# Kernel optimization log

Hardware: AMD Instinct MI355X
Metric: run time of the kernel (lower is better)

Reference implementation:

```python
import jax, jax.numpy as jnp
import numpy as np

N_NODES = 50000

def _gat_conv(x, src, dst, W, a_src, a_dst, bias, num_nodes, concat, neg_slope=0.2):
    # x: [N, Fin]; W: [Fin, H*C]; a_src/a_dst: [H, C]; src/dst: [E]
    H, C = a_src.shape
    h = (x @ W).reshape(-1, H, C)                      # [N, H, C]
    alpha_s = jnp.einsum('nhc,hc->nh', h, a_src)        # [N, H]
    alpha_d = jnp.einsum('nhc,hc->nh', h, a_dst)        # [N, H]
    e = alpha_s[src] + alpha_d[dst]                     # [E, H]
    e = jax.nn.leaky_relu(e, neg_slope)
    # segment softmax over destination nodes
    m = jax.ops.segment_max(e, dst, num_segments=num_nodes)   # [N, H]
    ex = jnp.exp(e - m[dst])                                   # [E, H]
    denom = jax.ops.segment_sum(ex, dst, num_segments=num_nodes)  # [N, H]
    alpha = ex / denom[dst]                                    # [E, H]
    msg = h[src] * alpha[:, :, None]                            # [E, H, C]
    out = jax.ops.segment_sum(msg, dst, num_segments=num_nodes)  # [N, H, C]
    if concat:
        out = out.reshape(-1, H * C)
    else:
        out = out.mean(axis=1)
    return out + bias

def _add_self_loops(edge_index, num_nodes):
    loop = jnp.arange(num_nodes, dtype=edge_index.dtype)
    src = jnp.concatenate([edge_index[0], loop])
    dst = jnp.concatenate([edge_index[1], loop])
    return src, dst

def setup_inputs() -> dict:
    key = jax.random.key(0)
    ks = jax.random.split(key, 12)
    N, E = N_NODES, 800000
    in_c, hid, out_c, H = 128, 32, 64, 4
    x = jax.random.normal(ks[0], (N, in_c), dtype=jnp.float32)
    edge_index = jax.random.randint(ks[1], (2, E), 0, N, dtype=jnp.int64)
    edge_weight = jax.random.uniform(ks[2], (E,), dtype=jnp.float32)
    s1 = 1.0 / np.sqrt(in_c)
    s2 = 1.0 / np.sqrt(hid * H)
    W1 = jax.random.normal(ks[3], (in_c, H * hid), dtype=jnp.float32) * s1
    a_src1 = jax.random.normal(ks[4], (H, hid), dtype=jnp.float32) * s1
    a_dst1 = jax.random.normal(ks[5], (H, hid), dtype=jnp.float32) * s1
    b1 = jnp.zeros((H * hid,), dtype=jnp.float32)
    W2 = jax.random.normal(ks[6], (H * hid, out_c), dtype=jnp.float32) * s2
    a_src2 = jax.random.normal(ks[7], (1, out_c), dtype=jnp.float32) * s2
    a_dst2 = jax.random.normal(ks[8], (1, out_c), dtype=jnp.float32) * s2
    b2 = jnp.zeros((out_c,), dtype=jnp.float32)
    return {"x": x, "edge_index": edge_index, "edge_weight": edge_weight,
            "W1": W1, "a_src1": a_src1, "a_dst1": a_dst1, "b1": b1,
            "W2": W2, "a_src2": a_src2, "a_dst2": a_dst2, "b2": b2}

def reference(x, edge_index, edge_weight, W1, a_src1, a_dst1, b1, W2, a_src2, a_dst2, b2):
    # PyG GATConv with edge_dim unset ignores edge_weight; self-loops added by default
    N = x.shape[0]
    src, dst = _add_self_loops(edge_index, N)
    h = _gat_conv(x, src, dst, W1, a_src1, a_dst1, b1, N, concat=True)
    h = jax.nn.relu(h)
    out = _gat_conv(h, src, dst, W2, a_src2, a_dst2, b2, N, concat=False)
    return out
```

## Files before the change

kernel.cpp:

```cpp
#include <hip/hip_runtime.h>
#include <hip/hip_fp16.h>
#include <math.h>


#define NEG_SLOPE 0.2f
#define NBLKA 256
#define MAXNB 512

__device__ __forceinline__ float leaky(float v) { return v > 0.f ? v : NEG_SLOPE * v; }

__global__ __launch_bounds__(256) void histc_k(const int* __restrict__ ei, int E, int ET,
                                               int* __restrict__ blkpref, int NB) {
  __shared__ int lhist[MAXNB];
  int chunk = (ET + NBLKA - 1) / NBLKA;
  int e0 = blockIdx.x * chunk, e1 = min(ET, e0 + chunk);
  for (int b = threadIdx.x; b < NB; b += 256) lhist[b] = 0;
  __syncthreads();
  for (int e = e0 + threadIdx.x; e < e1; e += 256) {
    int d = (e < E) ? ei[E + e] : (e - E);
    atomicAdd(&lhist[d >> 7], 1);
  }
  __syncthreads();
  for (int b = threadIdx.x; b < NB; b += 256)
    blkpref[b * NBLKA + blockIdx.x] = lhist[b];
}

__global__ __launch_bounds__(256) void scan_blk_k(int* __restrict__ blkpref,
                                                  int* __restrict__ bbase) {
  __shared__ int sm[NBLKA];
  int b = blockIdx.x, t = threadIdx.x;
  int v = blkpref[b * NBLKA + t];
  sm[t] = v;
  __syncthreads();
  #pragma unroll
  for (int off = 1; off < NBLKA; off <<= 1) {
    int x = (t >= off) ? sm[t - off] : 0;
    __syncthreads();
    sm[t] += x;
    __syncthreads();
  }
  blkpref[b * NBLKA + t] = sm[t] - v;
  if (t == NBLKA - 1) bbase[b] = sm[t];
}

__global__ __launch_bounds__(512) void scan_bkt_k(int* __restrict__ bbase,
                                                  int* __restrict__ lcnt,
                                                  int* __restrict__ rowptr,
                                                  int NB, int N, int ET) {
  __shared__ int sm[512];
  int t = threadIdx.x;
  int v = (t < NB) ? bbase[t] : 0;
  sm[t] = v;
  __syncthreads();
  #pragma unroll
  for (int off = 1; off < 512; off <<= 1) {
    int x = (t >= off) ? sm[t - off] : 0;
    __syncthreads();
    sm[t] += x;
    __syncthreads();
  }
  int excl = sm[t] - v;
  if (t <= NB) bbase[t] = excl;
  if (t == 0) { lcnt[0] = 0; lcnt[16] = 0; rowptr[N] = ET; }
}

__global__ __launch_bounds__(256) void passA_k(const int* __restrict__ ei, int E, int ET,
                                               const int* __restrict__ bbase,
                                               const int* __restrict__ blkpref,
                                               int* __restrict__ pairs, int NB) {
  __shared__ int lcur[MAXNB];
  int chunk = (ET + NBLKA - 1) / NBLKA;
  int e0 = blockIdx.x * chunk, e1 = min(ET, e0 + chunk);
  for (int b = threadIdx.x; b < NB; b += 256)
    lcur[b] = bbase[b] + blkpref[b * NBLKA + blockIdx.x];
  __syncthreads();
  for (int e = e0 + threadIdx.x; e < e1; e += 256) {
    int s, d;
    if (e < E) { s = ei[e]; d = ei[E + e]; } else { s = d = e - E; }
    int b = d >> 7;
    int pos = atomicAdd(&lcur[b], 1);
    pairs[pos] = ((d & 127) << 17) | s;
  }
}

__global__ __launch_bounds__(256) void passB_k(const int* __restrict__ pairs,
                                               const int* __restrict__ bbase,
                                               int* __restrict__ rowptr,
                                               int* __restrict__ srcs,
                                               int* __restrict__ small_list,
                                               int* __restrict__ big_list,
                                               int* __restrict__ lcnt, int N) {
  __shared__ int ncnt[128], spre[128], lcur[128];
  __shared__ int wcS[2], wcB[2], bS, bB;
  int b = blockIdx.x, t = threadIdx.x;
  int nb0 = b << 7;
  int nn = min(128, N - nb0);
  int e0 = bbase[b], e1 = bbase[b + 1];
  if (t < 128) ncnt[t] = 0;
  __syncthreads();
  for (int r = e0 + t; r < e1; r += 256)
    atomicAdd(&ncnt[pairs[r] >> 17], 1);
  __syncthreads();
  if (t < 128) spre[t] = ncnt[t];
  __syncthreads();
  #pragma unroll
  for (int off = 1; off < 128; off <<= 1) {
    int x = (t < 128 && t >= off) ? spre[t - off] : 0;
    __syncthreads();
    if (t < 128) spre[t] += x;
    __syncthreads();
  }
  if (t < nn) {
    int base = e0 + spre[t] - ncnt[t];
    rowptr[nb0 + t] = base;
    lcur[t] = base;
  }
  __syncthreads();
  for (int r = e0 + t; r < e1; r += 256) {
    int p = pairs[r];
    int pos = atomicAdd(&lcur[p >> 17], 1);
    srcs[pos] = p & 0x1FFFF;
  }
  int lane = t & 63, wv = t >> 6;
  bool valid = (t < nn);
  int deg = valid ? ncnt[t] : 0;
  bool isS = valid && (deg <= 16);
  bool isB = valid && (deg > 16);
  unsigned long long ms = __ballot(isS);
  unsigned long long mb = __ballot(isB);
  if (lane == 0 && wv < 2) { wcS[wv] = __popcll(ms); wcB[wv] = __popcll(mb); }
  __syncthreads();
  if (t == 0) {
    bS = atomicAdd(&lcnt[0],  wcS[0] + wcS[1]);
    bB = atomicAdd(&lcnt[16], wcB[0] + wcB[1]);
  }
  __syncthreads();
  unsigned long long below = (lane == 0) ? 0ull : (~0ull >> (64 - lane));
  int offS = bS + ((wv == 1) ? wcS[0] : 0);
  int offB = bB + ((wv == 1) ? wcB[0] : 0);
  if (isS) small_list[offS + __popcll(ms & below)] = nb0 + t;
  if (isB) big_list[offB + __popcll(mb & below)]   = nb0 + t;
}

__global__ __launch_bounds__(256) void gemm1_k(const float* __restrict__ X,
                                               const float* __restrict__ W,
                                               const float* __restrict__ aw_s,
                                               const float* __restrict__ aw_d,
                                               __half* __restrict__ Hh,
                                               float* __restrict__ as,
                                               float* __restrict__ ad, int N) {
  __shared__ float wl[32 * 128];
  __shared__ float xt[32][72];
  int cl = threadIdx.x & 31, rg = threadIdx.x >> 5;
  int c4 = cl * 4;
  int n0 = blockIdx.x * 64;
  float acc[8][4] = {};
  const float4* X4 = (const float4*)X;
  const float4* W4 = (const float4*)W;
  for (int k0 = 0; k0 < 128; k0 += 32) {
    __syncthreads();
    for (int i = threadIdx.x; i < 1024; i += 256)
      ((float4*)wl)[i] = W4[k0 * 32 + i];
    for (int i = threadIdx.x; i < 512; i += 256) {
      int r = i >> 3, kk4 = (i & 7) * 4;
      int n = n0 + r;
      float4 xv = (n < N) ? X4[(size_t)n * 32 + (k0 >> 2) + (i & 7)]
                          : make_float4(0.f, 0.f, 0.f, 0.f);
      xt[kk4 + 0][r] = xv.x; xt[kk4 + 1][r] = xv.y;
      xt[kk4 + 2][r] = xv.z; xt[kk4 + 3][r] = xv.w;
    }
    __syncthreads();
    #pragma unroll 8
    for (int kk = 0; kk < 32; ++kk) {
      float4 w4 = *(const float4*)&wl[kk * 128 + c4];
      float4 xa = *(const float4*)&xt[kk][rg * 8];
      float4 xb = *(const float4*)&xt[kk][rg * 8 + 4];
      float xr[8] = {xa.x, xa.y, xa.z, xa.w, xb.x, xb.y, xb.z, xb.w};
      #pragma unroll
      for (int j = 0; j < 8; ++j) {
        acc[j][0] += xr[j] * w4.x; acc[j][1] += xr[j] * w4.y;
        acc[j][2] += xr[j] * w4.z; acc[j][3] += xr[j] * w4.w;
      }
    }
  }
  float4 aws = *(const float4*)&aw_s[c4];
  float4 awd = *(const float4*)&aw_d[c4];
  #pragma unroll
  for (int j = 0; j < 8; ++j) {
    int n = n0 + rg * 8 + j;
    float ps = acc[j][0] * aws.x + acc[j][1] * aws.y + acc[j][2] * aws.z + acc[j][3] * aws.w;
    float pd = acc[j][0] * awd.x + acc[j][1] * awd.y + acc[j][2] * awd.z + acc[j][3] * awd.w;
    ps += __shfl_xor(ps, 1); ps += __shfl_xor(ps, 2); ps += __shfl_xor(ps, 4);
    pd += __shfl_xor(pd, 1); pd += __shfl_xor(pd, 2); pd += __shfl_xor(pd, 4);
    if (n < N) {
      __half2 p0 = __floats2half2_rn(acc[j][0], acc[j][1]);
      __half2 p1 = __floats2half2_rn(acc[j][2], acc[j][3]);
      __half2* dst = (__half2*)&Hh[(size_t)n * 128 + c4];
      dst[0] = p0; dst[1] = p1;
      if ((cl & 7) == 0) {
        as[n * 4 + (cl >> 3)] = ps;
        ad[n * 4 + (cl >> 3)] = pd;
      }
    }
  }
}

__global__ __launch_bounds__(256) void gemm2_k(const float* __restrict__ X,
                                               const float* __restrict__ W,
                                               const float* __restrict__ aw_s,
                                               const float* __restrict__ aw_d,
                                               __half* __restrict__ Hh,
                                               float* __restrict__ as,
                                               float* __restrict__ ad, int N) {
  __shared__ float wl[32 * 64];
  __shared__ float xt[32][72];
  int cl = threadIdx.x & 15, rg = threadIdx.x >> 4;
  int c4 = cl * 4;
  int n0 = blockIdx.x * 64;
  float acc[4][4] = {};
  const float4* X4 = (const float4*)X;
  const float4* W4 = (const float4*)W;
  for (int k0 = 0; k0 < 128; k0 += 32) {
    __syncthreads();
    for (int i = threadIdx.x; i < 512; i += 256)
      ((float4*)wl)[i] = W4[k0 * 16 + i];
    for (int i = threadIdx.x; i < 512; i += 256) {
      int r = i >> 3, kk4 = (i & 7) * 4;
      int n = n0 + r;
      float4 xv = (n < N) ? X4[(size_t)n * 32 + (k0 >> 2) + (i & 7)]
                          : make_float4(0.f, 0.f, 0.f, 0.f);
      xt[kk4 + 0][r] = xv.x; xt[kk4 + 1][r] = xv.y;
      xt[kk4 + 2][r] = xv.z; xt[kk4 + 3][r] = xv.w;
    }
    __syncthreads();
    #pragma unroll 8
    for (int kk = 0; kk < 32; ++kk) {
      float4 w4 = *(const float4*)&wl[kk * 64 + c4];
      float4 xa = *(const float4*)&xt[kk][rg * 4];
      float xr[4] = {xa.x, xa.y, xa.z, xa.w};
      #pragma unroll
      for (int j = 0; j < 4; ++j) {
        acc[j][0] += xr[j] * w4.x; acc[j][1] += xr[j] * w4.y;
        acc[j][2] += xr[j] * w4.z; acc[j][3] += xr[j] * w4.w;
      }
    }
  }
  float4 aws = *(const float4*)&aw_s[c4];
  float4 awd = *(const float4*)&aw_d[c4];
  #pragma unroll
  for (int j = 0; j < 4; ++j) {
    int n = n0 + rg * 4 + j;
    float ps = acc[j][0] * aws.x + acc[j][1] * aws.y + acc[j][2] * aws.z + acc[j][3] * aws.w;
    float pd = acc[j][0] * awd.x + acc[j][1] * awd.y + acc[j][2] * awd.z + acc[j][3] * awd.w;
    ps += __shfl_xor(ps, 1); ps += __shfl_xor(ps, 2);
    ps += __shfl_xor(ps, 4); ps += __shfl_xor(ps, 8);
    pd += __shfl_xor(pd, 1); pd += __shfl_xor(pd, 2);
    pd += __shfl_xor(pd, 4); pd += __shfl_xor(pd, 8);
    if (n < N) {
      __half2 p0 = __floats2half2_rn(acc[j][0], acc[j][1]);
      __half2 p1 = __floats2half2_rn(acc[j][2], acc[j][3]);
      __half2* dst = (__half2*)&Hh[(size_t)n * 64 + c4];
      dst[0] = p0; dst[1] = p1;
      if (cl == 0) { as[n] = ps; ad[n] = pd; }
    }
  }
}

__device__ __forceinline__ void load8h(const __half* p, float* f) {
  uint4 hv = *(const uint4*)p;
  float2 f0 = __half22float2(*(const __half2*)&hv.x);
  float2 f1 = __half22float2(*(const __half2*)&hv.y);
  float2 f2 = __half22float2(*(const __half2*)&hv.z);
  float2 f3 = __half22float2(*(const __half2*)&hv.w);
  f[0] = f0.x; f[1] = f0.y; f[2] = f1.x; f[3] = f1.y;
  f[4] = f2.x; f[5] = f2.y; f[6] = f3.x; f[7] = f3.y;
}

__global__ __launch_bounds__(256) void agg1_small_k(const int* __restrict__ rowptr,
                                                    const int* __restrict__ srcs,
                                                    const float* __restrict__ as,
                                                    const float* __restrict__ ad,
                                                    const __half* __restrict__ Hm,
                                                    const float* __restrict__ bias,
                                                    float* __restrict__ out,
                                                    const int* __restrict__ small_list,
                                                    const int* __restrict__ lcnt) {
  __shared__ float al_sm[16][17][4];
  __shared__ int   sr_sm[16][16];
  int g  = threadIdx.x >> 4;
  int gl = threadIdx.x & 15;
  int gidx = blockIdx.x * 16 + g;
  if (gidx >= lcnt[0]) return;
  int n = small_list[gidx];
  int r0 = rowptr[n];
  int deg = rowptr[n + 1] - r0;
  float4 adn = *(const float4*)&ad[n * 4];

  float e0 = -INFINITY, e1 = -INFINITY, e2 = -INFINITY, e3 = -INFINITY;
  int s = 0;
  if (gl < deg) {
    s = srcs[r0 + gl];
    float4 av = *(const float4*)&as[s * 4];
    e0 = leaky(av.x + adn.x); e1 = leaky(av.y + adn.y);
    e2 = leaky(av.z + adn.z); e3 = leaky(av.w + adn.w);
  }
  sr_sm[g][gl] = s;
  float m0 = e0, m1 = e1, m2 = e2, m3 = e3;
  #pragma unroll
  for (int off = 8; off > 0; off >>= 1) {
    m0 = fmaxf(m0, __shfl_xor(m0, off, 16)); m1 = fmaxf(m1, __shfl_xor(m1, off, 16));
    m2 = fmaxf(m2, __shfl_xor(m2, off, 16)); m3 = fmaxf(m3, __shfl_xor(m3, off, 16));
  }
  float sc0 = (gl < deg) ? __expf(e0 - m0) : 0.f;
  float sc1 = (gl < deg) ? __expf(e1 - m1) : 0.f;
  float sc2 = (gl < deg) ? __expf(e2 - m2) : 0.f;
  float sc3 = (gl < deg) ? __expf(e3 - m3) : 0.f;
  float s0 = sc0, s1 = sc1, s2 = sc2, s3 = sc3;
  #pragma unroll
  for (int off = 8; off > 0; off >>= 1) {
    s0 += __shfl_xor(s0, off, 16); s1 += __shfl_xor(s1, off, 16);
    s2 += __shfl_xor(s2, off, 16); s3 += __shfl_xor(s3, off, 16);
  }
  *(float4*)&al_sm[g][gl][0] =
      make_float4(sc0 / s0, sc1 / s1, sc2 / s2, sc3 / s3);

  int h = gl >> 2;
  int cbase = gl * 8;
  float a0 = 0.f, a1 = 0.f, a2 = 0.f, a3 = 0.f,
        a4 = 0.f, a5 = 0.f, a6 = 0.f, a7 = 0.f;
  for (int j = 0; j < deg; j += 4) {
    #pragma unroll
    for (int u = 0; u < 4; ++u) {
      int idx = j + u;
      bool vU = idx < deg;
      int jj = vU ? idx : 0;
      int   sU  = sr_sm[g][jj];
      float alU = vU ? al_sm[g][jj][h] : 0.f;
      float f[8];
      load8h(&Hm[(size_t)sU * 128 + cbase], f);
      a0 += f[0] * alU; a1 += f[1] * alU; a2 += f[2] * alU; a3 += f[3] * alU;
      a4 += f[4] * alU; a5 += f[5] * alU; a6 += f[6] * alU; a7 += f[7] * alU;
    }
  }
  float4 b0 = *(const float4*)&bias[cbase];
  float4 b1 = *(const float4*)&bias[cbase + 4];
  float4 o0, o1;
  o0.x = fmaxf(a0 + b0.x, 0.f); o0.y = fmaxf(a1 + b0.y, 0.f);
  o0.z = fmaxf(a2 + b0.z, 0.f); o0.w = fmaxf(a3 + b0.w, 0.f);
  o1.x = fmaxf(a4 + b1.x, 0.f); o1.y = fmaxf(a5 + b1.y, 0.f);
  o1.z = fmaxf(a6 + b1.z, 0.f); o1.w = fmaxf(a7 + b1.w, 0.f);
  *(float4*)&out[(size_t)n * 128 + cbase] = o0;
  *(float4*)&out[(size_t)n * 128 + cbase + 4] = o1;
}

__global__ __launch_bounds__(256) void agg1_big_k(const int* __restrict__ rowptr,
                                                  const int* __restrict__ srcs,
                                                  const float* __restrict__ as,
                                                  const float* __restrict__ ad,
                                                  const __half* __restrict__ Hm,
                                                  const float* __restrict__ bias,
                                                  float* __restrict__ out,
                                                  const int* __restrict__ big_list,
                                                  const int* __restrict__ lcnt) {
  __shared__ float al_sm[4][64][4];
  __shared__ int   sr_sm[4][64];
  int wv = threadIdx.x >> 6, lane = threadIdx.x & 63;
  int widx = blockIdx.x * 4 + wv;
  if (widx >= lcnt[16]) return;
  int n = big_list[widx];
  int r0 = rowptr[n], r1 = rowptr[n + 1];
  int deg = r1 - r0;
  int grp = lane >> 4, gl = lane & 15, h = gl >> 2;
  int cbase = gl * 8;
  float4 adn = *(const float4*)&ad[n * 4];

  float a0 = 0.f, a1 = 0.f, a2 = 0.f, a3 = 0.f,
        a4 = 0.f, a5 = 0.f, a6 = 0.f, a7 = 0.f;

  if (deg <= 64) {
    float e0 = -INFINITY, e1 = -INFINITY, e2 = -INFINITY, e3 = -INFINITY;
    int s = 0;
    if (lane < deg) {
      s = srcs[r0 + lane];
      float4 av = *(const float4*)&as[s * 4];
      e0 = leaky(av.x + adn.x); e1 = leaky(av.y + adn.y);
      e2 = leaky(av.z + adn.z); e3 = leaky(av.w + adn.w);
    }
    sr_sm[wv][lane] = s;
    float m0 = e0, m1 = e1, m2 = e2, m3 = e3;
    #pragma unroll
    for (int off = 32; off > 0; off >>= 1) {
      m0 = fmaxf(m0, __shfl_xor(m0, off)); m1 = fmaxf(m1, __shfl_xor(m1, off));
      m2 = fmaxf(m2, __shfl_xor(m2, off)); m3 = fmaxf(m3, __shfl_xor(m3, off));
    }
    float sc0 = (lane < deg) ? __expf(e0 - m0) : 0.f;
    float sc1 = (lane < deg) ? __expf(e1 - m1) : 0.f;
    float sc2 = (lane < deg) ? __expf(e2 - m2) : 0.f;
    float sc3 = (lane < deg) ? __expf(e3 - m3) : 0.f;
    float s0 = sc0, s1 = sc1, s2 = sc2, s3 = sc3;
    #pragma unroll
    for (int off = 32; off > 0; off >>= 1) {
      s0 += __shfl_xor(s0, off); s1 += __shfl_xor(s1, off);
      s2 += __shfl_xor(s2, off); s3 += __shfl_xor(s3, off);
    }
    *(float4*)&al_sm[wv][lane][0] =
        make_float4(sc0 / s0, sc1 / s1, sc2 / s2, sc3 / s3);

    for (int base = 0; base < deg; base += 16) {
      #pragma unroll
      for (int u = 0; u < 4; ++u) {
        int idx = base + grp * 4 + u;
        bool vU = idx < deg;
        int jj = vU ? idx : 0;
        int   sU  = sr_sm[wv][jj];
        float alU = vU ? al_sm[wv][jj][h] : 0.f;
        float f[8];
        load8h(&Hm[(size_t)sU * 128 + cbase], f);
        a0 += f[0] * alU; a1 += f[1] * alU; a2 += f[2] * alU; a3 += f[3] * alU;
        a4 += f[4] * alU; a5 += f[5] * alU; a6 += f[6] * alU; a7 += f[7] * alU;
      }
    }
  } else {
    float m0 = -INFINITY, m1 = -INFINITY, m2 = -INFINITY, m3 = -INFINITY;
    for (int r = r0 + lane; r < r1; r += 64) {
      int s = srcs[r];
      float4 av = *(const float4*)&as[s * 4];
      m0 = fmaxf(m0, leaky(av.x + adn.x)); m1 = fmaxf(m1, leaky(av.y + adn.y));
      m2 = fmaxf(m2, leaky(av.z + adn.z)); m3 = fmaxf(m3, leaky(av.w + adn.w));
    }
    #pragma unroll
    for (int off = 32; off > 0; off >>= 1) {
      m0 = fmaxf(m0, __shfl_xor(m0, off)); m1 = fmaxf(m1, __shfl_xor(m1, off));
      m2 = fmaxf(m2, __shfl_xor(m2, off)); m3 = fmaxf(m3, __shfl_xor(m3, off));
    }
    float s0 = 0.f, s1 = 0.f, s2 = 0.f, s3 = 0.f;
    for (int r = r0 + lane; r < r1; r += 64) {
      int s = srcs[r];
      float4 av = *(const float4*)&as[s * 4];
      s0 += __expf(leaky(av.x + adn.x) - m0); s1 += __expf(leaky(av.y + adn.y) - m1);
      s2 += __expf(leaky(av.z + adn.z) - m2); s3 += __expf(leaky(av.w + adn.w) - m3);
    }
    #pragma unroll
    for (int off = 32; off > 0; off >>= 1) {
      s0 += __shfl_xor(s0, off); s1 += __shfl_xor(s1, off);
      s2 += __shfl_xor(s2, off); s3 += __shfl_xor(s3, off);
    }
    float mhh = (h == 0) ? m0 : (h == 1) ? m1 : (h == 2) ? m2 : m3;
    float inv = 1.f / ((h == 0) ? s0 : (h == 1) ? s1 : (h == 2) ? s2 : s3);
    float adh = (h == 0) ? adn.x : (h == 1) ? adn.y : (h == 2) ? adn.z : adn.w;
    for (int r = r0; r < r1; r += 8) {
      int rA = r + grp, rB = rA + 4;
      bool vA = rA < r1, vB = rB < r1;
      int sA = srcs[vA ? rA : r0];
      int sB = srcs[vB ? rB : r0];
      float avA = as[sA * 4 + h], avB = as[sB * 4 + h];
      float alA = vA ? (__expf(leaky(avA + adh) - mhh) * inv) : 0.f;
      float alB = vB ? (__expf(leaky(avB + adh) - mhh) * inv) : 0.f;
      float fA[8], fB[8];
      load8h(&Hm[(size_t)sA * 128 + cbase], fA);
      load8h(&Hm[(size_t)sB * 128 + cbase], fB);
      a0 += fA[0] * alA + fB[0] * alB; a1 += fA[1] * alA + fB[1] * alB;
      a2 += fA[2] * alA + fB[2] * alB; a3 += fA[3] * alA + fB[3] * alB;
      a4 += fA[4] * alA + fB[4] * alB; a5 += fA[5] * alA + fB[5] * alB;
      a6 += fA[6] * alA + fB[6] * alB; a7 += fA[7] * alA + fB[7] * alB;
    }
  }
  a0 += __shfl_xor(a0, 16); a0 += __shfl_xor(a0, 32);
  a1 += __shfl_xor(a1, 16); a1 += __shfl_xor(a1, 32);
  a2 += __shfl_xor(a2, 16); a2 += __shfl_xor(a2, 32);
  a3 += __shfl_xor(a3, 16); a3 += __shfl_xor(a3, 32);
  a4 += __shfl_xor(a4, 16); a4 += __shfl_xor(a4, 32);
  a5 += __shfl_xor(a5, 16); a5 += __shfl_xor(a5, 32);
  a6 += __shfl_xor(a6, 16); a6 += __shfl_xor(a6, 32);
  a7 += __shfl_xor(a7, 16); a7 += __shfl_xor(a7, 32);
  if (grp == 0) {
    float4 b0 = *(const float4*)&bias[cbase];
    float4 b1 = *(const float4*)&bias[cbase + 4];
    float4 o0, o1;
    o0.x = fmaxf(a0 + b0.x, 0.f); o0.y = fmaxf(a1 + b0.y, 0.f);
    o0.z = fmaxf(a2 + b0.z, 0.f); o0.w = fmaxf(a3 + b0.w, 0.f);
    o1.x = fmaxf(a4 + b1.x, 0.f); o1.y = fmaxf(a5 + b1.y, 0.f);
    o1.z = fmaxf(a6 + b1.z, 0.f); o1.w = fmaxf(a7 + b1.w, 0.f);
    *(float4*)&out[(size_t)n * 128 + cbase] = o0;
    *(float4*)&out[(size_t)n * 128 + cbase + 4] = o1;
  }
}

__global__ __launch_bounds__(256) void agg2_small_k(const int* __restrict__ rowptr,
                                                    const int* __restrict__ srcs,
                                                    const float* __restrict__ as,
                                                    const float* __restrict__ ad,
                                                    const __half* __restrict__ Hm,
                                                    const float* __restrict__ bias,
                                                    float* __restrict__ out,
                                                    const int* __restrict__ small_list,
                                                    const int* __restrict__ lcnt) {
  __shared__ float al_sm[16][17];
  __shared__ int   sr_sm[16][16];
  int g  = threadIdx.x >> 4;
  int gl = threadIdx.x & 15;
  int gidx = blockIdx.x * 16 + g;
  if (gidx >= lcnt[0]) return;
  int n = small_list[gidx];
  int r0 = rowptr[n];
  int deg = rowptr[n + 1] - r0;
  float adn = ad[n];

  float e = -INFINITY;
  int s = 0;
  if (gl < deg) { s = srcs[r0 + gl]; e = leaky(as[s] + adn); }
  sr_sm[g][gl] = s;
  float m = e;
  #pragma unroll
  for (int off = 8; off > 0; off >>= 1) m = fmaxf(m, __shfl_xor(m, off, 16));
  float sc = (gl < deg) ? __expf(e - m) : 0.f;
  float ssum = sc;
  #pragma unroll
  for (int off = 8; off > 0; off >>= 1) ssum += __shfl_xor(ssum, off, 16);
  al_sm[g][gl] = sc / ssum;

  int cbase = gl * 4;
  float a0 = 0.f, a1 = 0.f, a2 = 0.f, a3 = 0.f;
  for (int j = 0; j < deg; j += 4) {
    #pragma unroll
    for (int u = 0; u < 4; ++u) {
      int idx = j + u;
      bool vU = idx < deg;
      int jj = vU ? idx : 0;
      int   sU  = sr_sm[g][jj];
      float alU = vU ? al_sm[g][jj] : 0.f;
      uint2 hv = *(const uint2*)&Hm[(size_t)sU * 64 + cbase];
      float2 f0 = __half22float2(*(const __half2*)&hv.x);
      float2 f1 = __half22float2(*(const __half2*)&hv.y);
      a0 += f0.x * alU; a1 += f0.y * alU; a2 += f1.x * alU; a3 += f1.y * alU;
    }
  }
  float4 bv = *(const float4*)&bias[cbase];
  float4 o;
  o.x = a0 + bv.x; o.y = a1 + bv.y; o.z = a2 + bv.z; o.w = a3 + bv.w;
  *(float4*)&out[(size_t)n * 64 + cbase] = o;
}

__global__ __launch_bounds__(256) void agg2_big_k(const int* __restrict__ rowptr,
                                                  const int* __restrict__ srcs,
                                                  const float* __restrict__ as,
                                                  const float* __restrict__ ad,
                                                  const __half* __restrict__ Hm,
                                                  const float* __restrict__ bias,
                                                  float* __restrict__ out,
                                                  const int* __restrict__ big_list,
                                                  const int* __restrict__ lcnt) {
  __shared__ float al_sm[4][64];
  __shared__ int   sr_sm[4][64];
  int wv = threadIdx.x >> 6, lane = threadIdx.x & 63;
  int widx = blockIdx.x * 4 + wv;
  if (widx >= lcnt[16]) return;
  int n = big_list[widx];
  int r0 = rowptr[n], r1 = rowptr[n + 1];
  int deg = r1 - r0;
  int grp = lane >> 4, gl = lane & 15;
  int cbase = gl * 4;
  float adn = ad[n];

  float a0 = 0.f, a1 = 0.f, a2 = 0.f, a3 = 0.f;

  if (deg <= 64) {
    float e = -INFINITY;
    int s = 0;
    if (lane < deg) { s = srcs[r0 + lane]; e = leaky(as[s] + adn); }
    sr_sm[wv][lane] = s;
    float m = e;
    #pragma unroll
    for (int off = 32; off > 0; off >>= 1) m = fmaxf(m, __shfl_xor(m, off));
    float sc = (lane < deg) ? __expf(e - m) : 0.f;
    float ssum = sc;
    #pragma unroll
    for (int off = 32; off > 0; off >>= 1) ssum += __shfl_xor(ssum, off);
    al_sm[wv][lane] = sc / ssum;

    for (int base = 0; base < deg; base += 16) {
      #pragma unroll
      for (int u = 0; u < 4; ++u) {
        int idx = base + grp * 4 + u;
        bool vU = idx < deg;
        int jj = vU ? idx : 0;
        int   sU  = sr_sm[wv][jj];
        float alU = vU ? al_sm[wv][jj] : 0.f;
        uint2 hv = *(const uint2*)&Hm[(size_t)sU * 64 + cbase];
        float2 f0 = __half22float2(*(const __half2*)&hv.x);
        float2 f1 = __half22float2(*(const __half2*)&hv.y);
        a0 += f0.x * alU; a1 += f0.y * alU; a2 += f1.x * alU; a3 += f1.y * alU;
      }
    }
  } else {
    float mh = -INFINITY;
    for (int r = r0 + lane; r < r1; r += 64)
      mh = fmaxf(mh, leaky(as[srcs[r]] + adn));
    #pragma unroll
    for (int off = 32; off > 0; off >>= 1) mh = fmaxf(mh, __shfl_xor(mh, off));
    float ssum = 0.f;
    for (int r = r0 + lane; r < r1; r += 64)
      ssum += __expf(leaky(as[srcs[r]] + adn) - mh);
    #pragma unroll
    for (int off = 32; off > 0; off >>= 1) ssum += __shfl_xor(ssum, off);
    float inv = 1.f / ssum;
    for (int r = r0; r < r1; r += 8) {
      int rA = r + grp, rB = rA + 4;
      bool vA = rA < r1, vB = rB < r1;
      int sA = srcs[vA ? rA : r0];
      int sB = srcs[vB ? rB : r0];
      float alA = vA ? (__expf(leaky(as[sA] + adn) - mh) * inv) : 0.f;
      float alB = vB ? (__expf(leaky(as[sB] + adn) - mh) * inv) : 0.f;
      uint2 hvA = *(const uint2*)&Hm[(size_t)sA * 64 + cbase];
      uint2 hvB = *(const uint2*)&Hm[(size_t)sB * 64 + cbase];
      float2 fA0 = __half22float2(*(const __half2*)&hvA.x);
      float2 fA1 = __half22float2(*(const __half2*)&hvA.y);
      float2 fB0 = __half22float2(*(const __half2*)&hvB.x);
      float2 fB1 = __half22float2(*(const __half2*)&hvB.y);
      a0 += fA0.x * alA + fB0.x * alB; a1 += fA0.y * alA + fB0.y * alB;
      a2 += fA1.x * alA + fB1.x * alB; a3 += fA1.y * alA + fB1.y * alB;
    }
  }
  a0 += __shfl_xor(a0, 16); a0 += __shfl_xor(a0, 32);
  a1 += __shfl_xor(a1, 16); a1 += __shfl_xor(a1, 32);
  a2 += __shfl_xor(a2, 16); a2 += __shfl_xor(a2, 32);
  a3 += __shfl_xor(a3, 16); a3 += __shfl_xor(a3, 32);
  if (grp == 0) {
    float4 bv = *(const float4*)&bias[cbase];
    float4 o;
    o.x = a0 + bv.x; o.y = a1 + bv.y; o.z = a2 + bv.z; o.w = a3 + bv.w;
    *(float4*)&out[(size_t)n * 64 + cbase] = o;
  }
}

extern "C" void kernel_launch(void* const* d_in, const int* in_sizes, int n_in,
                              void* d_out, int out_size, void* d_ws, size_t ws_size,
                              hipStream_t stream) {
  const float* x   = (const float*)d_in[0];
  const int*   ei  = (const int*)d_in[1];
  const float* W1  = (const float*)d_in[3];
  const float* aS1 = (const float*)d_in[4];
  const float* aD1 = (const float*)d_in[5];
  const float* b1  = (const float*)d_in[6];
  const float* W2  = (const float*)d_in[7];
  const float* aS2 = (const float*)d_in[8];
  const float* aD2 = (const float*)d_in[9];
  const float* b2  = (const float*)d_in[10];

  const int N  = in_sizes[0] / 128;
  const int E  = in_sizes[2];
  const int ET = E + N;
  const int NB = (N + 127) >> 7;

  float* ws   = (float*)d_ws;
  __half* h1h = (__half*)ws;
  float* out1 = ws + (size_t)N * 64;
  float* as1  = out1 + (size_t)N * 128;
  float* ad1  = as1  + (size_t)4 * N;
  float* as2  = ad1  + (size_t)4 * N;
  float* ad2  = as2  + (size_t)N;
  int*   lcnt    = (int*)(ad2 + (size_t)N);
  int*   rowptr  = lcnt + 32;
  int*   bbase   = rowptr + N + 1;
  int*   blkpref = bbase + NB + 1;
  int*   small_list = blkpref + NB * NBLKA;
  int*   big_list   = small_list + N;
  int*   srcs   = big_list + N;
  int*   pairs  = (int*)ws;
  __half* h2h  = h1h;
  float* out  = (float*)d_out;

  const int gb  = (N + 63) / 64;
  const int sb  = (N + 15) / 16;
  const int bb  = (N + 3) / 4;

  histc_k<<<NBLKA, 256, 0, stream>>>(ei, E, ET, blkpref, NB);
  scan_blk_k<<<NB, 256, 0, stream>>>(blkpref, bbase);
  scan_bkt_k<<<1, 512, 0, stream>>>(bbase, lcnt, rowptr, NB, N, ET);
  passA_k<<<NBLKA, 256, 0, stream>>>(ei, E, ET, bbase, blkpref, pairs, NB);
  passB_k<<<NB, 256, 0, stream>>>(pairs, bbase, rowptr, srcs,
                                  small_list, big_list, lcnt, N);

  gemm1_k<<<gb, 256, 0, stream>>>(x, W1, aS1, aD1, h1h, as1, ad1, N);
  agg1_small_k<<<sb, 256, 0, stream>>>(rowptr, srcs, as1, ad1, h1h, b1, out1,
                                       small_list, lcnt);
  agg1_big_k<<<bb, 256, 0, stream>>>(rowptr, srcs, as1, ad1, h1h, b1, out1,
                                     big_list, lcnt);

  gemm2_k<<<gb, 256, 0, stream>>>(out1, W2, aS2, aD2, h2h, as2, ad2, N);
  agg2_small_k<<<sb, 256, 0, stream>>>(rowptr, srcs, as2, ad2, h2h, b2, out,
                                       small_list, lcnt);
  agg2_big_k<<<bb, 256, 0, stream>>>(rowptr, srcs, as2, ad2, h2h, b2, out,
                                     big_list, lcnt);
}
```

Baseline: 243.9 us.

## Merge small/big aggregation kernels and store layer-1 output in fp16

The separate small-degree and big-degree aggregation kernels for each layer are merged into one launch, with blocks below SB taking the small path and the rest the big path. This removes two kernel launches and lets both node classes run at the same time. The layer-1 activation is now written as fp16 and read back by gemm2 as fp16, which halves that intermediate's write and read traffic at some cost in precision.

```diff
diff --git a/kernel.cpp b/kernel.cpp
--- a/kernel.cpp
+++ b/kernel.cpp
@@ -193,10 +193,9 @@
     ps += __shfl_xor(ps, 1); ps += __shfl_xor(ps, 2); ps += __shfl_xor(ps, 4);
     pd += __shfl_xor(pd, 1); pd += __shfl_xor(pd, 2); pd += __shfl_xor(pd, 4);
     if (n < N) {
-      __half2 p0 = __floats2half2_rn(acc[j][0], acc[j][1]);
-      __half2 p1 = __floats2half2_rn(acc[j][2], acc[j][3]);
       __half2* dst = (__half2*)&Hh[(size_t)n * 128 + c4];
-      dst[0] = p0; dst[1] = p1;
+      dst[0] = __floats2half2_rn(acc[j][0], acc[j][1]);
+      dst[1] = __floats2half2_rn(acc[j][2], acc[j][3]);
       if ((cl & 7) == 0) {
         as[n * 4 + (cl >> 3)] = ps;
         ad[n * 4 + (cl >> 3)] = pd;
@@ -205,7 +204,7 @@
   }
 }
 
-__global__ __launch_bounds__(256) void gemm2_k(const float* __restrict__ X,
+__global__ __launch_bounds__(256) void gemm2_k(const __half* __restrict__ X,
                                                const float* __restrict__ W,
                                                const float* __restrict__ aw_s,
                                                const float* __restrict__ aw_d,
@@ -218,19 +217,25 @@
   int c4 = cl * 4;
   int n0 = blockIdx.x * 64;
   float acc[4][4] = {};
-  const float4* X4 = (const float4*)X;
+  const uint4* X8 = (const uint4*)X;
   const float4* W4 = (const float4*)W;
   for (int k0 = 0; k0 < 128; k0 += 32) {
     __syncthreads();
     for (int i = threadIdx.x; i < 512; i += 256)
       ((float4*)wl)[i] = W4[k0 * 16 + i];
-    for (int i = threadIdx.x; i < 512; i += 256) {
-      int r = i >> 3, kk4 = (i & 7) * 4;
+    for (int i = threadIdx.x; i < 256; i += 256) {
+      int r = i >> 2, kk8 = (i & 3) * 8;
       int n = n0 + r;
-      float4 xv = (n < N) ? X4[(size_t)n * 32 + (k0 >> 2) + (i & 7)]
-                          : make_float4(0.f, 0.f, 0.f, 0.f);
-      xt[kk4 + 0][r] = xv.x; xt[kk4 + 1][r] = xv.y;
-      xt[kk4 + 2][r] = xv.z; xt[kk4 + 3][r] = xv.w;
+      uint4 hv = (n < N) ? X8[(size_t)n * 16 + (k0 >> 3) + (i & 3)]
+                         : make_uint4(0, 0, 0, 0);
+      float2 f0 = __half22float2(*(const __half2*)&hv.x);
+      float2 f1 = __half22float2(*(const __half2*)&hv.y);
+      float2 f2 = __half22float2(*(const __half2*)&hv.z);
+      float2 f3 = __half22float2(*(const __half2*)&hv.w);
+      xt[kk8 + 0][r] = f0.x; xt[kk8 + 1][r] = f0.y;
+      xt[kk8 + 2][r] = f1.x; xt[kk8 + 3][r] = f1.y;
+      xt[kk8 + 4][r] = f2.x; xt[kk8 + 5][r] = f2.y;
+      xt[kk8 + 6][r] = f3.x; xt[kk8 + 7][r] = f3.y;
     }
     __syncthreads();
     #pragma unroll 8
@@ -257,10 +262,9 @@
     pd += __shfl_xor(pd, 1); pd += __shfl_xor(pd, 2);
     pd += __shfl_xor(pd, 4); pd += __shfl_xor(pd, 8);
     if (n < N) {
-      __half2 p0 = __floats2half2_rn(acc[j][0], acc[j][1]);
-      __half2 p1 = __floats2half2_rn(acc[j][2], acc[j][3]);
       __half2* dst = (__half2*)&Hh[(size_t)n * 64 + c4];
-      dst[0] = p0; dst[1] = p1;
+      dst[0] = __floats2half2_rn(acc[j][0], acc[j][1]);
+      dst[1] = __floats2half2_rn(acc[j][2], acc[j][3]);
       if (cl == 0) { as[n] = ps; ad[n] = pd; }
     }
   }
@@ -276,96 +280,87 @@
   f[4] = f2.x; f[5] = f2.y; f[6] = f3.x; f[7] = f3.y;
 }
 
-__global__ __launch_bounds__(256) void agg1_small_k(const int* __restrict__ rowptr,
-                                                    const int* __restrict__ srcs,
-                                                    const float* __restrict__ as,
-                                                    const float* __restrict__ ad,
-                                                    const __half* __restrict__ Hm,
-                                                    const float* __restrict__ bias,
-                                                    float* __restrict__ out,
-                                                    const int* __restrict__ small_list,
-                                                    const int* __restrict__ lcnt) {
-  __shared__ float al_sm[16][17][4];
-  __shared__ int   sr_sm[16][16];
-  int g  = threadIdx.x >> 4;
-  int gl = threadIdx.x & 15;
-  int gidx = blockIdx.x * 16 + g;
-  if (gidx >= lcnt[0]) return;
-  int n = small_list[gidx];
-  int r0 = rowptr[n];
-  int deg = rowptr[n + 1] - r0;
-  float4 adn = *(const float4*)&ad[n * 4];
-
-  float e0 = -INFINITY, e1 = -INFINITY, e2 = -INFINITY, e3 = -INFINITY;
-  int s = 0;
-  if (gl < deg) {
-    s = srcs[r0 + gl];
-    float4 av = *(const float4*)&as[s * 4];
-    e0 = leaky(av.x + adn.x); e1 = leaky(av.y + adn.y);
-    e2 = leaky(av.z + adn.z); e3 = leaky(av.w + adn.w);
-  }
-  sr_sm[g][gl] = s;
-  float m0 = e0, m1 = e1, m2 = e2, m3 = e3;
-  #pragma unroll
-  for (int off = 8; off > 0; off >>= 1) {
-    m0 = fmaxf(m0, __shfl_xor(m0, off, 16)); m1 = fmaxf(m1, __shfl_xor(m1, off, 16));
-    m2 = fmaxf(m2, __shfl_xor(m2, off, 16)); m3 = fmaxf(m3, __shfl_xor(m3, off, 16));
-  }
-  float sc0 = (gl < deg) ? __expf(e0 - m0) : 0.f;
-  float sc1 = (gl < deg) ? __expf(e1 - m1) : 0.f;
-  float sc2 = (gl < deg) ? __expf(e2 - m2) : 0.f;
-  float sc3 = (gl < deg) ? __expf(e3 - m3) : 0.f;
-  float s0 = sc0, s1 = sc1, s2 = sc2, s3 = sc3;
-  #pragma unroll
-  for (int off = 8; off > 0; off >>= 1) {
-    s0 += __shfl_xor(s0, off, 16); s1 += __shfl_xor(s1, off, 16);
-    s2 += __shfl_xor(s2, off, 16); s3 += __shfl_xor(s3, off, 16);
-  }
-  *(float4*)&al_sm[g][gl][0] =
-      make_float4(sc0 / s0, sc1 / s1, sc2 / s2, sc3 / s3);
-
-  int h = gl >> 2;
-  int cbase = gl * 8;
-  float a0 = 0.f, a1 = 0.f, a2 = 0.f, a3 = 0.f,
-        a4 = 0.f, a5 = 0.f, a6 = 0.f, a7 = 0.f;
-  for (int j = 0; j < deg; j += 4) {
-    #pragma unroll
-    for (int u = 0; u < 4; ++u) {
-      int idx = j + u;
-      bool vU = idx < deg;
-      int jj = vU ? idx : 0;
-      int   sU  = sr_sm[g][jj];
-      float alU = vU ? al_sm[g][jj][h] : 0.f;
-      float f[8];
-      load8h(&Hm[(size_t)sU * 128 + cbase], f);
-      a0 += f[0] * alU; a1 += f[1] * alU; a2 += f[2] * alU; a3 += f[3] * alU;
-      a4 += f[4] * alU; a5 += f[5] * alU; a6 += f[6] * alU; a7 += f[7] * alU;
-    }
-  }
-  float4 b0 = *(const float4*)&bias[cbase];
-  float4 b1 = *(const float4*)&bias[cbase + 4];
-  float4 o0, o1;
-  o0.x = fmaxf(a0 + b0.x, 0.f); o0.y = fmaxf(a1 + b0.y, 0.f);
-  o0.z = fmaxf(a2 + b0.z, 0.f); o0.w = fmaxf(a3 + b0.w, 0.f);
-  o1.x = fmaxf(a4 + b1.x, 0.f); o1.y = fmaxf(a5 + b1.y, 0.f);
-  o1.z = fmaxf(a6 + b1.z, 0.f); o1.w = fmaxf(a7 + b1.w, 0.f);
-  *(float4*)&out[(size_t)n * 128 + cbase] = o0;
-  *(float4*)&out[(size_t)n * 128 + cbase + 4] = o1;
-}
-
-__global__ __launch_bounds__(256) void agg1_big_k(const int* __restrict__ rowptr,
-                                                  const int* __restrict__ srcs,
-                                                  const float* __restrict__ as,
-                                                  const float* __restrict__ ad,
-                                                  const __half* __restrict__ Hm,
-                                                  const float* __restrict__ bias,
-                                                  float* __restrict__ out,
-                                                  const int* __restrict__ big_list,
-                                                  const int* __restrict__ lcnt) {
+__global__ __launch_bounds__(256) void agg1_k(const int* __restrict__ rowptr,
+                                              const int* __restrict__ srcs,
+                                              const float* __restrict__ as,
+                                              const float* __restrict__ ad,
+                                              const __half* __restrict__ Hm,
+                                              const float* __restrict__ bias,
+                                              __half* __restrict__ out,
+                                              const int* __restrict__ small_list,
+                                              const int* __restrict__ big_list,
+                                              const int* __restrict__ lcnt, int SB) {
+  if (blockIdx.x < (unsigned)SB) {
+    __shared__ float al_sm[16][17][4];
+    __shared__ int   sr_sm[16][16];
+    int g  = threadIdx.x >> 4;
+    int gl = threadIdx.x & 15;
+    int gidx = blockIdx.x * 16 + g;
+    if (gidx >= lcnt[0]) return;
+    int n = small_list[gidx];
+    int r0 = rowptr[n];
+    int deg = rowptr[n + 1] - r0;
+    float4 adn = *(const float4*)&ad[n * 4];
+
+    float e0 = -INFINITY, e1 = -INFINITY, e2 = -INFINITY, e3 = -INFINITY;
+    int s = 0;
+    if (gl < deg) {
+      s = srcs[r0 + gl];
+      float4 av = *(const float4*)&as[s * 4];
+      e0 = leaky(av.x + adn.x); e1 = leaky(av.y + adn.y);
+      e2 = leaky(av.z + adn.z); e3 = leaky(av.w + adn.w);
+    }
+    sr_sm[g][gl] = s;
+    float m0 = e0, m1 = e1, m2 = e2, m3 = e3;
+    #pragma unroll
+    for (int off = 8; off > 0; off >>= 1) {
+      m0 = fmaxf(m0, __shfl_xor(m0, off, 16)); m1 = fmaxf(m1, __shfl_xor(m1, off, 16));
+      m2 = fmaxf(m2, __shfl_xor(m2, off, 16)); m3 = fmaxf(m3, __shfl_xor(m3, off, 16));
+    }
+    float sc0 = (gl < deg) ? __expf(e0 - m0) : 0.f;
+    float sc1 = (gl < deg) ? __expf(e1 - m1) : 0.f;
+    float sc2 = (gl < deg) ? __expf(e2 - m2) : 0.f;
+    float sc3 = (gl < deg) ? __expf(e3 - m3) : 0.f;
+    float s0 = sc0, s1 = sc1, s2 = sc2, s3 = sc3;
+    #pragma unroll
+    for (int off = 8; off > 0; off >>= 1) {
+      s0 += __shfl_xor(s0, off, 16); s1 += __shfl_xor(s1, off, 16);
+      s2 += __shfl_xor(s2, off, 16); s3 += __shfl_xor(s3, off, 16);
+    }
+    *(float4*)&al_sm[g][gl][0] =
+        make_float4(sc0 / s0, sc1 / s1, sc2 / s2, sc3 / s3);
+
+    int h = gl >> 2;
+    int cbase = gl * 8;
+    float a0 = 0.f, a1 = 0.f, a2 = 0.f, a3 = 0.f,
+          a4 = 0.f, a5 = 0.f, a6 = 0.f, a7 = 0.f;
+    for (int j = 0; j < deg; j += 4) {
+      #pragma unroll
+      for (int u = 0; u < 4; ++u) {
+        int idx = j + u;
+        bool vU = idx < deg;
+        int jj = vU ? idx : 0;
+        int   sU  = sr_sm[g][jj];
+        float alU = vU ? al_sm[g][jj][h] : 0.f;
+        float f[8];
+        load8h(&Hm[(size_t)sU * 128 + cbase], f);
+        a0 += f[0] * alU; a1 += f[1] * alU; a2 += f[2] * alU; a3 += f[3] * alU;
+        a4 += f[4] * alU; a5 += f[5] * alU; a6 += f[6] * alU; a7 += f[7] * alU;
+      }
+    }
+    float4 b0 = *(const float4*)&bias[cbase];
+    float4 b1 = *(const float4*)&bias[cbase + 4];
+    __half2* dst = (__half2*)&out[(size_t)n * 128 + cbase];
+    dst[0] = __floats2half2_rn(fmaxf(a0 + b0.x, 0.f), fmaxf(a1 + b0.y, 0.f));
+    dst[1] = __floats2half2_rn(fmaxf(a2 + b0.z, 0.f), fmaxf(a3 + b0.w, 0.f));
+    dst[2] = __floats2half2_rn(fmaxf(a4 + b1.x, 0.f), fmaxf(a5 + b1.y, 0.f));
+    dst[3] = __floats2half2_rn(fmaxf(a6 + b1.z, 0.f), fmaxf(a7 + b1.w, 0.f));
+    return;
+  }
   __shared__ float al_sm[4][64][4];
   __shared__ int   sr_sm[4][64];
   int wv = threadIdx.x >> 6, lane = threadIdx.x & 63;
-  int widx = blockIdx.x * 4 + wv;
+  int widx = (blockIdx.x - SB) * 4 + wv;
   if (widx >= lcnt[16]) return;
   int n = big_list[widx];
   int r0 = rowptr[n], r1 = rowptr[n + 1];
@@ -476,84 +471,75 @@
   if (grp == 0) {
     float4 b0 = *(const float4*)&bias[cbase];
     float4 b1 = *(const float4*)&bias[cbase + 4];
-    float4 o0, o1;
-    o0.x = fmaxf(a0 + b0.x, 0.f); o0.y = fmaxf(a1 + b0.y, 0.f);
-    o0.z = fmaxf(a2 + b0.z, 0.f); o0.w = fmaxf(a3 + b0.w, 0.f);
-    o1.x = fmaxf(a4 + b1.x, 0.f); o1.y = fmaxf(a5 + b1.y, 0.f);
-    o1.z = fmaxf(a6 + b1.z, 0.f); o1.w = fmaxf(a7 + b1.w, 0.f);
-    *(float4*)&out[(size_t)n * 128 + cbase] = o0;
-    *(float4*)&out[(size_t)n * 128 + cbase + 4] = o1;
-  }
-}
-
-__global__ __launch_bounds__(256) void agg2_small_k(const int* __restrict__ rowptr,
-                                                    const int* __restrict__ srcs,
-                                                    const float* __restrict__ as,
-                                                    const float* __restrict__ ad,
-                                                    const __half* __restrict__ Hm,
-                                                    const float* __restrict__ bias,
-                                                    float* __restrict__ out,
-                                                    const int* __restrict__ small_list,
-                                                    const int* __restrict__ lcnt) {
-  __shared__ float al_sm[16][17];
-  __shared__ int   sr_sm[16][16];
-  int g  = threadIdx.x >> 4;
-  int gl = threadIdx.x & 15;
-  int gidx = blockIdx.x * 16 + g;
-  if (gidx >= lcnt[0]) return;
-  int n = small_list[gidx];
-  int r0 = rowptr[n];
-  int deg = rowptr[n + 1] - r0;
-  float adn = ad[n];
-
-  float e = -INFINITY;
-  int s = 0;
-  if (gl < deg) { s = srcs[r0 + gl]; e = leaky(as[s] + adn); }
-  sr_sm[g][gl] = s;
-  float m = e;
-  #pragma unroll
-  for (int off = 8; off > 0; off >>= 1) m = fmaxf(m, __shfl_xor(m, off, 16));
-  float sc = (gl < deg) ? __expf(e - m) : 0.f;
-  float ssum = sc;
-  #pragma unroll
-  for (int off = 8; off > 0; off >>= 1) ssum += __shfl_xor(ssum, off, 16);
-  al_sm[g][gl] = sc / ssum;
-
-  int cbase = gl * 4;
-  float a0 = 0.f, a1 = 0.f, a2 = 0.f, a3 = 0.f;
-  for (int j = 0; j < deg; j += 4) {
-    #pragma unroll
-    for (int u = 0; u < 4; ++u) {
-      int idx = j + u;
-      bool vU = idx < deg;
-      int jj = vU ? idx : 0;
-      int   sU  = sr_sm[g][jj];
-      float alU = vU ? al_sm[g][jj] : 0.f;
-      uint2 hv = *(const uint2*)&Hm[(size_t)sU * 64 + cbase];
-      float2 f0 = __half22float2(*(const __half2*)&hv.x);
-      float2 f1 = __half22float2(*(const __half2*)&hv.y);
-      a0 += f0.x * alU; a1 += f0.y * alU; a2 += f1.x * alU; a3 += f1.y * alU;
-    }
-  }
-  float4 bv = *(const float4*)&bias[cbase];
-  float4 o;
-  o.x = a0 + bv.x; o.y = a1 + bv.y; o.z = a2 + bv.z; o.w = a3 + bv.w;
-  *(float4*)&out[(size_t)n * 64 + cbase] = o;
-}
-
-__global__ __launch_bounds__(256) void agg2_big_k(const int* __restrict__ rowptr,
-                                                  const int* __restrict__ srcs,
-                                                  const float* __restrict__ as,
-                                                  const float* __restrict__ ad,
-                                                  const __half* __restrict__ Hm,
-                                                  const float* __restrict__ bias,
-                                                  float* __restrict__ out,
-                                                  const int* __restrict__ big_list,
-                                                  const int* __restrict__ lcnt) {
+    __half2* dst = (__half2*)&out[(size_t)n * 128 + cbase];
+    dst[0] = __floats2half2_rn(fmaxf(a0 + b0.x, 0.f), fmaxf(a1 + b0.y, 0.f));
+    dst[1] = __floats2half2_rn(fmaxf(a2 + b0.z, 0.f), fmaxf(a3 + b0.w, 0.f));
+    dst[2] = __floats2half2_rn(fmaxf(a4 + b1.x, 0.f), fmaxf(a5 + b1.y, 0.f));
+    dst[3] = __floats2half2_rn(fmaxf(a6 + b1.z, 0.f), fmaxf(a7 + b1.w, 0.f));
+  }
+}
+
+__global__ __launch_bounds__(256) void agg2_k(const int* __restrict__ rowptr,
+                                              const int* __restrict__ srcs,
+                                              const float* __restrict__ as,
+                                              const float* __restrict__ ad,
+                                              const __half* __restrict__ Hm,
+                                              const float* __restrict__ bias,
+                                              float* __restrict__ out,
+                                              const int* __restrict__ small_list,
+                                              const int* __restrict__ big_list,
+                                              const int* __restrict__ lcnt, int SB) {
+  if (blockIdx.x < (unsigned)SB) {
+    __shared__ float al_sm[16][17];
+    __shared__ int   sr_sm[16][16];
+    int g  = threadIdx.x >> 4;
+    int gl = threadIdx.x & 15;
+    int gidx = blockIdx.x * 16 + g;
+    if (gidx >= lcnt[0]) return;
+    int n = small_list[gidx];
+    int r0 = rowptr[n];
+    int deg = rowptr[n + 1] - r0;
+    float adn = ad[n];
+
+    float e = -INFINITY;
+    int s = 0;
+    if (gl < deg) { s = srcs[r0 + gl]; e = leaky(as[s] + adn); }
+    sr_sm[g][gl] = s;
+    float m = e;
+    #pragma unroll
+    for (int off = 8; off > 0; off >>= 1) m = fmaxf(m, __shfl_xor(m, off, 16));
+    float sc = (gl < deg) ? __expf(e - m) : 0.f;
+    float ssum = sc;
+    #pragma unroll
+    for (int off = 8; off > 0; off >>= 1) ssum += __shfl_xor(ssum, off, 16);
+    al_sm[g][gl] = sc / ssum;
+
+    int cbase = gl * 4;
+    float a0 = 0.f, a1 = 0.f, a2 = 0.f, a3 = 0.f;
+    for (int j = 0; j < deg; j += 4) {
+      #pragma unroll
+      for (int u = 0; u < 4; ++u) {
+        int idx = j + u;
+        bool vU = idx < deg;
+        int jj = vU ? idx : 0;
+        int   sU  = sr_sm[g][jj];
+        float alU = vU ? al_sm[g][jj] : 0.f;
+        uint2 hv = *(const uint2*)&Hm[(size_t)sU * 64 + cbase];
+        float2 f0 = __half22float2(*(const __half2*)&hv.x);
+        float2 f1 = __half22float2(*(const __half2*)&hv.y);
+        a0 += f0.x * alU; a1 += f0.y * alU; a2 += f1.x * alU; a3 += f1.y * alU;
+      }
+    }
+    float4 bv = *(const float4*)&bias[cbase];
+    float4 o;
+    o.x = a0 + bv.x; o.y = a1 + bv.y; o.z = a2 + bv.z; o.w = a3 + bv.w;
+    *(float4*)&out[(size_t)n * 64 + cbase] = o;
+    return;
+  }
   __shared__ float al_sm[4][64];
   __shared__ int   sr_sm[4][64];
   int wv = threadIdx.x >> 6, lane = threadIdx.x & 63;
-  int widx = blockIdx.x * 4 + wv;
+  int widx = (blockIdx.x - SB) * 4 + wv;
   if (widx >= lcnt[16]) return;
   int n = big_list[widx];
   int r0 = rowptr[n], r1 = rowptr[n + 1];
@@ -652,13 +638,13 @@
   const int ET = E + N;
   const int NB = (N + 127) >> 7;
 
-  float* ws   = (float*)d_ws;
-  __half* h1h = (__half*)ws;
-  float* out1 = ws + (size_t)N * 64;
-  float* as1  = out1 + (size_t)N * 128;
-  float* ad1  = as1  + (size_t)4 * N;
-  float* as2  = ad1  + (size_t)4 * N;
-  float* ad2  = as2  + (size_t)N;
+  float* ws    = (float*)d_ws;
+  __half* h1h  = (__half*)ws;
+  __half* o1h  = (__half*)(ws + (size_t)N * 64);
+  float* as1   = ws + (size_t)N * 128;
+  float* ad1   = as1  + (size_t)4 * N;
+  float* as2   = ad1  + (size_t)4 * N;
+  float* ad2   = as2  + (size_t)N;
   int*   lcnt    = (int*)(ad2 + (size_t)N);
   int*   rowptr  = lcnt + 32;
   int*   bbase   = rowptr + N + 1;
@@ -670,9 +656,9 @@
   __half* h2h  = h1h;
   float* out  = (float*)d_out;
 
-  const int gb  = (N + 63) / 64;
-  const int sb  = (N + 15) / 16;
-  const int bb  = (N + 3) / 4;
+  const int gb = (N + 63) / 64;
+  const int sb = (N + 15) / 16;
+  const int bb = (N + 3) / 4;
 
   histc_k<<<NBLKA, 256, 0, stream>>>(ei, E, ET, blkpref, NB);
   scan_blk_k<<<NB, 256, 0, stream>>>(blkpref, bbase);
@@ -682,14 +668,10 @@
                                   small_list, big_list, lcnt, N);
 
   gemm1_k<<<gb, 256, 0, stream>>>(x, W1, aS1, aD1, h1h, as1, ad1, N);
-  agg1_small_k<<<sb, 256, 0, stream>>>(rowptr, srcs, as1, ad1, h1h, b1, out1,
-                                       small_list, lcnt);
-  agg1_big_k<<<bb, 256, 0, stream>>>(rowptr, srcs, as1, ad1, h1h, b1, out1,
-                                     big_list, lcnt);
-
-  gemm2_k<<<gb, 256, 0, stream>>>(out1, W2, aS2, aD2, h2h, as2, ad2, N);
-  agg2_small_k<<<sb, 256, 0, stream>>>(rowptr, srcs, as2, ad2, h2h, b2, out,
-                                       small_list, lcnt);
-  agg2_big_k<<<bb, 256, 0, stream>>>(rowptr, srcs, as2, ad2, h2h, b2, out,
-                                     big_list, lcnt);
-}
+  agg1_k<<<sb + bb, 256, 0, stream>>>(rowptr, srcs, as1, ad1, h1h, b1, o1h,
+                                      small_list, big_list, lcnt, sb);
+
+  gemm2_k<<<gb, 256, 0, stream>>>(o1h, W2, aS2, aD2, h2h, as2, ad2, N);
+  agg2_k<<<sb + bb, 256, 0, stream>>>(rowptr, srcs, as2, ad2, h2h, b2, out,
+                                      small_list, big_list, lcnt, sb);
+}
```

Result: faster. 235.0 us (-3.7%).
